# Kernel tuning notes

Hardware: AMD Instinct MI355X
Metric: run time of the kernel (lower is better)

## Reference

```python
import jax, jax.numpy as jnp
import numpy as np

B, N, DEG = 128, 512, 16          # graphs, nodes/graph, avg degree
NB = B * N                        # 65536 nodes
E = NB * DEG                      # 1048576 edges
K1, K2, K3 = 410, 205, 103        # ceil(0.8*512), ceil(0.5*410), ceil(0.5*205)
H, C = 4, 32                      # GAT heads, head dim
F_IN, ED = 128, 7


def _glorot(key, shape, fan_in):
    return jax.random.normal(key, shape, dtype=jnp.float32) / np.float32(np.sqrt(fan_in))


def setup_inputs() -> dict:
    key = jax.random.key(0)
    ks = jax.random.split(key, 24)
    x = jax.random.normal(ks[0], (NB, F_IN), dtype=jnp.float32)
    # random intra-graph edges, then offset per graph
    src = jax.random.randint(ks[1], (E,), 0, N)
    dst = jax.random.randint(ks[2], (E,), 0, N)
    off = jnp.repeat(jnp.arange(B) * N, N * DEG)
    edge_index = jnp.stack([src + off, dst + off]).astype(jnp.int32)
    edge_attr = jax.random.normal(ks[3], (E, ED), dtype=jnp.float32)
    p = {
        'c1_wl': _glorot(ks[4], (F_IN, F_IN), F_IN), 'c1_bl': jnp.zeros((F_IN,), jnp.float32), 'c1_wr': _glorot(ks[5], (F_IN, F_IN), F_IN),
        'p1_w': _glorot(ks[6], (F_IN,), F_IN),
        'c2_wl': _glorot(ks[7], (F_IN, F_IN), F_IN), 'c2_bl': jnp.zeros((F_IN,), jnp.float32), 'c2_wr': _glorot(ks[8], (F_IN, F_IN), F_IN),
        'p2_wrel': _glorot(ks[9], (F_IN, 1), F_IN), 'p2_brel': jnp.zeros((1,), jnp.float32), 'p2_wroot': _glorot(ks[10], (F_IN, 1), F_IN),
        'g_w': _glorot(ks[11], (F_IN, H * C), F_IN), 'g_as': _glorot(ks[12], (H, C), C), 'g_ad': _glorot(ks[13], (H, C), C),
        'g_we': _glorot(ks[14], (ED, H * C), ED), 'g_ae': _glorot(ks[15], (H, C), C), 'g_b': jnp.zeros((H * C,), jnp.float32),
        'p3_wrel': _glorot(ks[16], (F_IN, 1), F_IN), 'p3_brel': jnp.zeros((1,), jnp.float32), 'p3_wroot': _glorot(ks[17], (F_IN, 1), F_IN),
        'l1_w': _glorot(ks[18], (F_IN, F_IN), F_IN), 'l1_b': jnp.zeros((F_IN,), jnp.float32),
        'l2_w': _glorot(ks[19], (F_IN, 64), F_IN), 'l2_b': jnp.zeros((64,), jnp.float32),
        'l3_w': _glorot(ks[20], (64, 1), 64), 'l3_b': jnp.zeros((1,), jnp.float32),
    }
    return {'x': x, 'edge_index': edge_index, 'edge_attr': edge_attr, **p}


def _sage(x, src, dst, emf, wl, bl, wr):
    # SAGEConv: mean-aggregate neighbors (masked edges), lin_l(agg)+lin_r(x)
    agg = jax.ops.segment_sum(x[src] * emf[:, None], dst, num_segments=NB)
    cnt = jax.ops.segment_sum(emf, dst, num_segments=NB)
    mean = agg / jnp.maximum(cnt, 1.0)[:, None]
    return mean @ wl + bl + x @ wr


def _graphconv(x, src, dst, emf, wrel, brel, wroot):
    # GraphConv (SAGPooling score GNN): add-aggregation
    agg = jax.ops.segment_sum(x[src] * emf[:, None], dst, num_segments=NB)
    return (agg @ wrel + brel + x @ wroot).reshape(-1)


def _pool(x, score, nmask, K):
    # per-graph static top-k (equal-size graphs) == PyG topk + filter
    masked = jnp.where(nmask, score, -jnp.inf).reshape(B, N)
    idx = jax.lax.top_k(masked, K)[1]
    nm = jnp.zeros((B, N), dtype=bool).at[jnp.arange(B)[:, None], idx].set(True).reshape(-1)
    x = jnp.where(nm[:, None], x * score[:, None], 0.0)
    return x, nm


def _gap(x, K):
    # global mean pool; dropped nodes are exactly zero, K live nodes per graph
    return x.reshape(B, N, F_IN).sum(axis=1) / K


def _gat(x, src, dst, emf, nmask, edge_attr, w, a_s, a_d, w_e, a_e, b):
    xs = (x @ w).reshape(NB, H, C)
    al_s = (xs * a_s).sum(-1)                                   # [NB,H]
    al_d = (xs * a_d).sum(-1)
    al_e = ((edge_attr @ w_e).reshape(E, H, C) * a_e).sum(-1)    # [E,H]
    alpha = jax.nn.leaky_relu(al_s[src] + al_d[dst] + al_e, 0.2)
    alpha = jnp.where(emf[:, None] > 0, alpha, -jnp.inf)
    # PyG add_self_loops=True with fill_value='mean' for edge_attr
    ea_mean = (edge_attr * emf[:, None]).sum(0) / jnp.maximum(emf.sum(), 1.0)
    al_se = ((ea_mean @ w_e).reshape(H, C) * a_e).sum(-1)        # [H]
    alpha_self = jax.nn.leaky_relu(al_s + al_d + al_se[None, :], 0.2)
    alpha_self = jnp.where(nmask[:, None], alpha_self, -jnp.inf)
    m = jnp.maximum(jax.ops.segment_max(alpha, dst, num_segments=NB), alpha_self)
    m = jnp.where(jnp.isfinite(m), m, 0.0)
    ex = jnp.exp(alpha - m[dst]) * emf[:, None]
    ex_s = jnp.where(nmask[:, None], jnp.exp(alpha_self - m), 0.0)
    den = jnp.maximum(jax.ops.segment_sum(ex, dst, num_segments=NB) + ex_s, 1e-16)
    num = jax.ops.segment_sum(ex[:, :, None] * xs[src], dst, num_segments=NB) + ex_s[:, :, None] * xs
    return (num / den[:, :, None]).reshape(NB, H * C) + b


def _forward(x, edge_index, edge_attr, c1_wl, c1_bl, c1_wr, p1_w, c2_wl, c2_bl, c2_wr,
             p2_wrel, p2_brel, p2_wroot, g_w, g_as, g_ad, g_we, g_ae, g_b,
             p3_wrel, p3_brel, p3_wroot, l1_w, l1_b, l2_w, l2_b, l3_w, l3_b):
    src, dst = edge_index[0], edge_index[1]
    nmask = jnp.ones((NB,), dtype=bool)
    emf = jnp.ones((E,), jnp.float32)

    # block 1: SAGEConv -> TopKPooling(0.8) -> gap
    x = jax.nn.relu(_sage(x, src, dst, emf, c1_wl, c1_bl, c1_wr))
    s1 = jnp.tanh((x @ p1_w) / jnp.linalg.norm(p1_w))
    x, nmask = _pool(x, s1, nmask, K1)
    emf = emf * nmask[src] * nmask[dst]
    x1 = _gap(x, K1)

    # block 2: SAGEConv -> SAGPooling(0.5) -> gap
    x = jax.nn.relu(_sage(x, src, dst, emf, c2_wl, c2_bl, c2_wr))
    s2 = jnp.tanh(_graphconv(x, src, dst, emf, p2_wrel, p2_brel, p2_wroot))
    x, nmask = _pool(x, s2, nmask, K2)
    emf = emf * nmask[src] * nmask[dst]
    x2 = _gap(x, K2)

    # block 3: GATConv(128->32x4, edge_dim=7) -> SAGPooling(0.5) -> gap
    x = jax.nn.relu(_gat(x, src, dst, emf, nmask, edge_attr, g_w, g_as, g_ad, g_we, g_ae, g_b))
    s3 = jnp.tanh(_graphconv(x, src, dst, emf, p3_wrel, p3_brel, p3_wroot))
    x, nmask = _pool(x, s3, nmask, K3)
    x3 = _gap(x, K3)

    h = x1 + x2 + x3
    h = jax.nn.relu(h @ l1_w + l1_b)
    h = jax.nn.relu(h @ l2_w + l2_b)   # dropout identity in eval
    return jax.nn.sigmoid(h @ l3_w + l3_b)[:, 0]


def reference(x, edge_index, edge_attr, c1_wl, c1_bl, c1_wr, p1_w, c2_wl, c2_bl, c2_wr,
              p2_wrel, p2_brel, p2_wroot, g_w, g_as, g_ad, g_we, g_ae, g_b,
              p3_wrel, p3_brel, p3_wroot, l1_w, l1_b, l2_w, l2_b, l3_w, l3_b):
    return _forward(x, edge_index, edge_attr, c1_wl, c1_bl, c1_wr, p1_w, c2_wl, c2_bl, c2_wr,
                    p2_wrel, p2_brel, p2_wroot, g_w, g_as, g_ad, g_we, g_ae, g_b,
                    p3_wrel, p3_brel, p3_wroot, l1_w, l1_b, l2_w, l2_b, l3_w, l3_b)
```

## Files before the change

kernel.cpp:

```cpp
#include <hip/hip_runtime.h>
#include <math.h>

#define NBV 65536
#define EV  1048576
#define BV  128
#define K1V 410
#define K2V 205
#define K3V 103
#define NEG_BIG (-1.0e38f)

__device__ __forceinline__ float lrelu(float x){ return x > 0.f ? x : 0.2f*x; }

__global__ void k_sentinel(float* out, float v){
  int i = threadIdx.x;
  if (i < 128) out[i] = v;
}

__global__ void k_fill1(float* p, int n){
  int i = blockIdx.x*blockDim.x + threadIdx.x;
  if (i < n) p[i] = 1.f;
}

__global__ void k_zero_i(int* p, int n){
  int i = blockIdx.x*blockDim.x + threadIdx.x;
  if (i < n) p[i] = 0;
}

__global__ void k_hist(const int* dst, int* dcnt){
  int e = blockIdx.x*blockDim.x + threadIdx.x;
  if (e < EV) atomicAdd(&dcnt[dst[e]], 1);
}

__global__ void k_scan1(const int* dcnt, int* rp, int* bsum){
  __shared__ int sc[256];
  int t = threadIdx.x, i = blockIdx.x*256 + t;
  int v = dcnt[i];
  sc[t] = v; __syncthreads();
  for (int o = 1; o < 256; o <<= 1){
    int x = (t >= o) ? sc[t-o] : 0;
    __syncthreads();
    sc[t] += x;
    __syncthreads();
  }
  rp[i] = sc[t];
  if (t == 255) bsum[blockIdx.x] = sc[t];
}

__global__ void k_scan2(int* bsum){
  __shared__ int sc[256];
  int t = threadIdx.x;
  int v = bsum[t];
  sc[t] = v; __syncthreads();
  for (int o = 1; o < 256; o <<= 1){
    int x = (t >= o) ? sc[t-o] : 0;
    __syncthreads();
    sc[t] += x;
    __syncthreads();
  }
  bsum[t] = sc[t] - v;
}

__global__ void k_scan3(int* rp, const int* dcnt, const int* bsum){
  int t = threadIdx.x, i = blockIdx.x*256 + t;
  rp[i] = rp[i] - dcnt[i] + bsum[blockIdx.x];
  if (i == 0) rp[NBV] = EV;
}

__global__ void k_scatter(const int* src, const int* dst, const int* rp, int* fill,
                          int* csr_src, int* csr_eid){
  int e = blockIdx.x*blockDim.x + threadIdx.x;
  if (e < EV){
    int d = dst[e];
    int pos = atomicAdd(&fill[d], 1);
    int slot = rp[d] + pos;
    csr_src[slot] = src[e];
    csr_eid[slot] = e;
  }
}

__global__ void k_invnorm(const float* wv, float* outv){
  __shared__ float sc[128];
  int t = threadIdx.x;
  float v = wv[t];
  sc[t] = v*v; __syncthreads();
  for (int o = 64; o > 0; o >>= 1){ if (t < o) sc[t] += sc[t+o]; __syncthreads(); }
  if (t == 0) outv[0] = 1.f / sqrtf(sc[0]);
}

__global__ void k_ve(const float* g_we, const float* g_ae, float* ve){
  int t = threadIdx.x;
  if (t < 28){
    int ed = t >> 2, h = t & 3;
    float a = 0.f;
    for (int c = 0; c < 32; c++) a += g_we[ed*128 + h*32 + c] * g_ae[h*32 + c];
    ve[t] = a;
  }
}

__global__ void k_ale(const float* ea, const float* ve, float* ALE){
  int e = blockIdx.x*blockDim.x + threadIdx.x;
  if (e < EV){
    float a0=0.f,a1=0.f,a2=0.f,a3=0.f;
    for (int ed = 0; ed < 7; ed++){
      float x = ea[e*7 + ed];
      a0 += x*ve[ed*4+0]; a1 += x*ve[ed*4+1]; a2 += x*ve[ed*4+2]; a3 += x*ve[ed*4+3];
    }
    float4 o; o.x=a0; o.y=a1; o.z=a2; o.w=a3;
    *(float4*)&ALE[(size_t)e*4] = o;
  }
}

__global__ void __launch_bounds__(256) k_sage_agg(const float* X, const float* nmask,
    const int* rp, const int* csr_src, float* AGG, int masked){
  int g = blockIdx.x & 127;
  int blk = blockIdx.x >> 7;
  int i = g*512 + blk*8 + (threadIdx.x >> 5);
  int c4 = threadIdx.x & 31;
  float ax=0.f,ay=0.f,az=0.f,aw=0.f,cnt=0.f;
  if (!masked || nmask[i] > 0.f){
    int r0 = rp[i], r1 = rp[i+1];
    int s = r0;
    for (; s + 4 <= r1; s += 4){
      int sn0 = csr_src[s+0], sn1 = csr_src[s+1], sn2 = csr_src[s+2], sn3 = csr_src[s+3];
      float4 v0 = *(const float4*)&X[((size_t)sn0 << 7) + (c4 << 2)];
      float4 v1 = *(const float4*)&X[((size_t)sn1 << 7) + (c4 << 2)];
      float4 v2 = *(const float4*)&X[((size_t)sn2 << 7) + (c4 << 2)];
      float4 v3 = *(const float4*)&X[((size_t)sn3 << 7) + (c4 << 2)];
      float nm0 = masked ? nmask[sn0] : 1.f;
      float nm1 = masked ? nmask[sn1] : 1.f;
      float nm2 = masked ? nmask[sn2] : 1.f;
      float nm3 = masked ? nmask[sn3] : 1.f;
      if (nm0 > 0.f){ ax += v0.x; ay += v0.y; az += v0.z; aw += v0.w; cnt += 1.f; }
      if (nm1 > 0.f){ ax += v1.x; ay += v1.y; az += v1.z; aw += v1.w; cnt += 1.f; }
      if (nm2 > 0.f){ ax += v2.x; ay += v2.y; az += v2.z; aw += v2.w; cnt += 1.f; }
      if (nm3 > 0.f){ ax += v3.x; ay += v3.y; az += v3.z; aw += v3.w; cnt += 1.f; }
    }
    for (; s < r1; s++){
      int sn = csr_src[s];
      float nm = masked ? nmask[sn] : 1.f;
      if (nm > 0.f){
        const float4 v = *(const float4*)&X[((size_t)sn << 7) + (c4 << 2)];
        ax += v.x; ay += v.y; az += v.z; aw += v.w; cnt += 1.f;
      }
    }
  }
  float inv = 1.f / fmaxf(cnt, 1.f);
  float4 o; o.x = ax*inv; o.y = ay*inv; o.z = az*inv; o.w = aw*inv;
  *(float4*)&AGG[((size_t)i << 7) + (c4 << 2)] = o;
}

__global__ void __launch_bounds__(512) k_gemm(const float* A1, const float* A2,
    const float* W1, const float* W2, const float* bias,
    float* OUT, int has2, int relu, int hasb){
  __shared__ float ws[128][128];
  __shared__ float as[16][136];
  int t = threadIdx.x;
  int n0 = blockIdx.x * 128;
  int rowg = t >> 5;
  int colg = t & 31;
  int rb = rowg * 8;
  int jb = colg * 4;
  int an = t >> 2;
  int ak = (t & 3) << 2;
  float acc[8][4];
  for (int r = 0; r < 8; r++)
    for (int j = 0; j < 4; j++) acc[r][j] = 0.f;
  int nmat = has2 ? 2 : 1;
  for (int m = 0; m < nmat; m++){
    const float* A = (m == 0) ? A1 : A2;
    const float* W = (m == 0) ? W1 : W2;
    __syncthreads();
    for (int ii = 0; ii < 8; ii++){
      int idx4 = t + 512*ii;
      int kk = idx4 >> 5;
      int jj = (idx4 & 31) << 2;
      *(float4*)&ws[kk][jj] = *(const float4*)&W[kk*128 + jj];
    }
    float4 rA = *(const float4*)&A[((size_t)(n0+an) << 7) + ak];
    for (int c = 0; c < 8; c++){
      if (c > 0) __syncthreads();
      as[ak+0][an] = rA.x;
      as[ak+1][an] = rA.y;
      as[ak+2][an] = rA.z;
      as[ak+3][an] = rA.w;
      __syncthreads();
      if (c+1 < 8)
        rA = *(const float4*)&A[((size_t)(n0+an) << 7) + (c+1)*16 + ak];
      int kb = c*16;
      for (int kk = 0; kk < 16; kk++){
        float4 wv = *(const float4*)&ws[kb+kk][jb];
        float4 aL = *(const float4*)&as[kk][rb];
        float4 aH = *(const float4*)&as[kk][rb+4];
        float a0=aL.x,a1=aL.y,a2=aL.z,a3=aL.w,a4=aH.x,a5=aH.y,a6=aH.z,a7=aH.w;
        acc[0][0]+=a0*wv.x; acc[0][1]+=a0*wv.y; acc[0][2]+=a0*wv.z; acc[0][3]+=a0*wv.w;
        acc[1][0]+=a1*wv.x; acc[1][1]+=a1*wv.y; acc[1][2]+=a1*wv.z; acc[1][3]+=a1*wv.w;
        acc[2][0]+=a2*wv.x; acc[2][1]+=a2*wv.y; acc[2][2]+=a2*wv.z; acc[2][3]+=a2*wv.w;
        acc[3][0]+=a3*wv.x; acc[3][1]+=a3*wv.y; acc[3][2]+=a3*wv.z; acc[3][3]+=a3*wv.w;
        acc[4][0]+=a4*wv.x; acc[4][1]+=a4*wv.y; acc[4][2]+=a4*wv.z; acc[4][3]+=a4*wv.w;
        acc[5][0]+=a5*wv.x; acc[5][1]+=a5*wv.y; acc[5][2]+=a5*wv.z; acc[5][3]+=a5*wv.w;
        acc[6][0]+=a6*wv.x; acc[6][1]+=a6*wv.y; acc[6][2]+=a6*wv.z; acc[6][3]+=a6*wv.w;
        acc[7][0]+=a7*wv.x; acc[7][1]+=a7*wv.y; acc[7][2]+=a7*wv.z; acc[7][3]+=a7*wv.w;
      }
    }
  }
  float bj0=0.f,bj1=0.f,bj2=0.f,bj3=0.f;
  if (hasb){
    bj0 = bias[jb+0]; bj1 = bias[jb+1]; bj2 = bias[jb+2]; bj3 = bias[jb+3];
  }
  for (int r = 0; r < 8; r++){
    float4 o;
    o.x = acc[r][0]+bj0; o.y = acc[r][1]+bj1; o.z = acc[r][2]+bj2; o.w = acc[r][3]+bj3;
    if (relu){
      o.x = fmaxf(o.x,0.f); o.y = fmaxf(o.y,0.f); o.z = fmaxf(o.z,0.f); o.w = fmaxf(o.w,0.f);
    }
    *(float4*)&OUT[((size_t)(n0+rb+r) << 7) + jb] = o;
  }
}

__global__ void __launch_bounds__(256) k_score1(const float* X, const float* pw, const float* invn, float* s){
  int gid = blockIdx.x*256 + threadIdx.x;
  int i = gid >> 5, c4 = gid & 31;
  float4 v = *(const float4*)&X[((size_t)i << 7) + (c4 << 2)];
  float4 wv = *(const float4*)&pw[c4 << 2];
  float a = v.x*wv.x + v.y*wv.y + v.z*wv.z + v.w*wv.w;
  for (int o = 16; o > 0; o >>= 1) a += __shfl_down(a, o, 32);
  if (c4 == 0) s[i] = tanhf(a * invn[0]);
}

__global__ void __launch_bounds__(256) k_qr(const float* X, const float* wrel, const float* wroot,
                                            float* q, float* r){
  int gid = blockIdx.x*256 + threadIdx.x;
  int i = gid >> 5, c4 = gid & 31;
  float4 v = *(const float4*)&X[((size_t)i << 7) + (c4 << 2)];
  float4 wa = *(const float4*)&wrel[c4 << 2];
  float4 wb = *(const float4*)&wroot[c4 << 2];
  float aq = v.x*wa.x + v.y*wa.y + v.z*wa.z + v.w*wa.w;
  float ar = v.x*wb.x + v.y*wb.y + v.z*wb.z + v.w*wb.w;
  for (int o = 16; o > 0; o >>= 1){
    aq += __shfl_down(aq, o, 32);
    ar += __shfl_down(ar, o, 32);
  }
  if (c4 == 0){ q[i] = aq; r[i] = ar; }
}

__global__ void k_gconv(const float* q, const float* r, const float* nmask,
    const int* rp, const int* csr_src, const float* brel, float* s){
  int i = blockIdx.x*blockDim.x + threadIdx.x;
  if (i >= NBV) return;
  float acc = 0.f;
  if (nmask[i] > 0.f){
    int r0 = rp[i], r1 = rp[i+1];
    int t2 = r0;
    for (; t2 + 4 <= r1; t2 += 4){
      int sn0 = csr_src[t2+0], sn1 = csr_src[t2+1], sn2 = csr_src[t2+2], sn3 = csr_src[t2+3];
      float nm0 = nmask[sn0], nm1 = nmask[sn1], nm2 = nmask[sn2], nm3 = nmask[sn3];
      float q0 = q[sn0], q1 = q[sn1], q2 = q[sn2], q3 = q[sn3];
      if (nm0 > 0.f) acc += q0;
      if (nm1 > 0.f) acc += q1;
      if (nm2 > 0.f) acc += q2;
      if (nm3 > 0.f) acc += q3;
    }
    for (; t2 < r1; t2++){
      int sn = csr_src[t2];
      if (nmask[sn] > 0.f) acc += q[sn];
    }
  }
  s[i] = tanhf(acc + brel[0] + r[i]);
}

__global__ void __launch_bounds__(512) k_pool(const float* s, float* nmask, float* sel, int K){
  __shared__ float sc[512];
  int b = blockIdx.x, t = threadIdx.x;
  int i = b*512 + t;
  float nm = nmask[i];
  float sv = s[i];
  float ms = (nm > 0.f) ? sv : NEG_BIG;
  sc[t] = ms;
  __syncthreads();
  int rank = 0;
  for (int j = 0; j < 512; j++){
    float o = sc[j];
    rank += ((o > ms) || (o == ms && j < t)) ? 1 : 0;
  }
  bool selb = rank < K;
  nmask[i] = selb ? 1.f : 0.f;
  sel[i] = selb ? sv : 0.f;
}

__global__ void __launch_bounds__(128) k_scale_part(float* X, const float* sel, float* part){
  int b = blockIdx.x >> 3, q = blockIdx.x & 7, c = threadIdx.x;
  float acc = 0.f;
  for (int n = q*64; n < q*64 + 64; n++){
    int i = b*512 + n;
    float v = X[((size_t)i << 7) + c] * sel[i];
    X[((size_t)i << 7) + c] = v;
    acc += v;
  }
  part[(size_t)blockIdx.x*128 + c] = acc;
}

__global__ void __launch_bounds__(128) k_gap_final(const float* part, float* gap, float invK){
  int b = blockIdx.x, c = threadIdx.x;
  float s = 0.f;
  for (int q = 0; q < 8; q++) s += part[(size_t)(b*8+q)*128 + c];
  gap[b*128 + c] = s * invK;
}

__global__ void k_heads(const float* xs, const float* a_s, const float* a_d,
                        float* alS, float* alD){
  int gid = blockIdx.x*blockDim.x + threadIdx.x;
  int i = gid >> 2, h = gid & 3;
  if (i >= NBV) return;
  const float4* xr = (const float4*)&xs[((size_t)i << 7) + h*32];
  const float4* wa = (const float4*)&a_s[h*32];
  const float4* wd = (const float4*)&a_d[h*32];
  float as_ = 0.f, ad_ = 0.f;
  for (int c4 = 0; c4 < 8; c4++){
    float4 v = xr[c4]; float4 A = wa[c4]; float4 D = wd[c4];
    as_ += v.x*A.x + v.y*A.y + v.z*A.z + v.w*A.w;
    ad_ += v.x*D.x + v.y*D.y + v.z*D.z + v.w*D.w;
  }
  alS[gid] = as_; alD[gid] = ad_;
}

__global__ void __launch_bounds__(256) k_ea_part(const float* ea, const int* srcA, const int* dstA,
    const float* nmask, float* part){
  float p[8] = {0.f,0.f,0.f,0.f,0.f,0.f,0.f,0.f};
  for (int e = blockIdx.x*256 + threadIdx.x; e < EV; e += 256*256){
    if (nmask[srcA[e]] > 0.f && nmask[dstA[e]] > 0.f){
      for (int d = 0; d < 7; d++) p[d] += ea[e*7 + d];
      p[7] += 1.f;
    }
  }
  __shared__ float red[256];
  for (int comp = 0; comp < 8; comp++){
    red[threadIdx.x] = p[comp]; __syncthreads();
    for (int o = 128; o > 0; o >>= 1){ if (threadIdx.x < o) red[threadIdx.x] += red[threadIdx.x + o]; __syncthreads(); }
    if (threadIdx.x == 0) part[blockIdx.x*8 + comp] = red[0];
    __syncthreads();
  }
}

__global__ void k_ea_final(const float* part, float* easum){
  int h = threadIdx.x;
  if (h < 8){
    float s = 0.f;
    for (int b = 0; b < 256; b++) s += part[b*8 + h];
    easum[h] = s;
  }
}

__global__ void k_alse(const float* easum, const float* ve, float* alse){
  if (threadIdx.x == 0 && blockIdx.x == 0){
    float cnt = fmaxf(easum[7], 1.f);
    for (int h = 0; h < 4; h++){
      float s = 0.f;
      for (int ed = 0; ed < 7; ed++) s += (easum[ed]/cnt) * ve[ed*4 + h];
      alse[h] = s;
    }
  }
}

__global__ void __launch_bounds__(256) k_gat(const float* xs, const float* alS, const float* alD,
    const float* ALE, const float* nmask, const int* rp, const int* csr_src,
    const int* csr_eid, const float* alse, const float* g_b, float* OUT){
  int g = blockIdx.x & 127;
  int blk = blockIdx.x >> 7;
  int i = g*512 + blk*8 + (threadIdx.x >> 5);
  int lane = threadIdx.x & 31;
  int h = lane >> 3;
  int cidx = h*8 + (lane & 7);
  float nmi = nmask[i];
  const float4* xs4 = (const float4*)xs;
  float m = 0.f, den = 0.f;
  float4 acc; acc.x=0.f; acc.y=0.f; acc.z=0.f; acc.w=0.f;
  if (nmi > 0.f){
    float ald_i = alD[i*4 + h];
    m = lrelu(alS[i*4 + h] + ald_i + alse[h]);
    den = 1.f;
    acc = xs4[(size_t)i*32 + cidx];
    int r0 = rp[i], r1 = rp[i+1];
    int s = r0;
    for (; s + 4 <= r1; s += 4){
      int sn0 = csr_src[s+0], sn1 = csr_src[s+1], sn2 = csr_src[s+2], sn3 = csr_src[s+3];
      int e0 = csr_eid[s+0], e1 = csr_eid[s+1], e2 = csr_eid[s+2], e3 = csr_eid[s+3];
      float nm0 = nmask[sn0], nm1 = nmask[sn1], nm2 = nmask[sn2], nm3 = nmask[sn3];
      float al0 = alS[sn0*4 + h], al1 = alS[sn1*4 + h], al2 = alS[sn2*4 + h], al3 = alS[sn3*4 + h];
      float ae0 = ALE[(size_t)e0*4 + h], ae1 = ALE[(size_t)e1*4 + h];
      float ae2 = ALE[(size_t)e2*4 + h], ae3 = ALE[(size_t)e3*4 + h];
      float4 v0 = xs4[(size_t)sn0*32 + cidx];
      float4 v1 = xs4[(size_t)sn1*32 + cidx];
      float4 v2 = xs4[(size_t)sn2*32 + cidx];
      float4 v3 = xs4[(size_t)sn3*32 + cidx];
      if (nm0 > 0.f){
        float a = lrelu(al0 + ald_i + ae0);
        float mn = fmaxf(m, a); float pm = expf(m - mn); float pa = expf(a - mn);
        den = den*pm + pa;
        acc.x = acc.x*pm + pa*v0.x; acc.y = acc.y*pm + pa*v0.y;
        acc.z = acc.z*pm + pa*v0.z; acc.w = acc.w*pm + pa*v0.w;
        m = mn;
      }
      if (nm1 > 0.f){
        float a = lrelu(al1 + ald_i + ae1);
        float mn = fmaxf(m, a); float pm = expf(m - mn); float pa = expf(a - mn);
        den = den*pm + pa;
        acc.x = acc.x*pm + pa*v1.x; acc.y = acc.y*pm + pa*v1.y;
        acc.z = acc.z*pm + pa*v1.z; acc.w = acc.w*pm + pa*v1.w;
        m = mn;
      }
      if (nm2 > 0.f){
        float a = lrelu(al2 + ald_i + ae2);
        float mn = fmaxf(m, a); float pm = expf(m - mn); float pa = expf(a - mn);
        den = den*pm + pa;
        acc.x = acc.x*pm + pa*v2.x; acc.y = acc.y*pm + pa*v2.y;
        acc.z = acc.z*pm + pa*v2.z; acc.w = acc.w*pm + pa*v2.w;
        m = mn;
      }
      if (nm3 > 0.f){
        float a = lrelu(al3 + ald_i + ae3);
        float mn = fmaxf(m, a); float pm = expf(m - mn); float pa = expf(a - mn);
        den = den*pm + pa;
        acc.x = acc.x*pm + pa*v3.x; acc.y = acc.y*pm + pa*v3.y;
        acc.z = acc.z*pm + pa*v3.z; acc.w = acc.w*pm + pa*v3.w;
        m = mn;
      }
    }
    for (; s < r1; s++){
      int sn = csr_src[s];
      if (nmask[sn] > 0.f){
        float a = lrelu(alS[sn*4 + h] + ald_i + ALE[(size_t)csr_eid[s]*4 + h]);
        float4 v = xs4[(size_t)sn*32 + cidx];
        float mn = fmaxf(m, a); float pm = expf(m - mn); float pa = expf(a - mn);
        den = den*pm + pa;
        acc.x = acc.x*pm + pa*v.x; acc.y = acc.y*pm + pa*v.y;
        acc.z = acc.z*pm + pa*v.z; acc.w = acc.w*pm + pa*v.w;
        m = mn;
      }
    }
  }
  den = fmaxf(den, 1e-16f);
  float rd = 1.f/den;
  int cb = cidx << 2;
  float4 o;
  o.x = fmaxf(acc.x*rd + g_b[cb+0], 0.f);
  o.y = fmaxf(acc.y*rd + g_b[cb+1], 0.f);
  o.z = fmaxf(acc.z*rd + g_b[cb+2], 0.f);
  o.w = fmaxf(acc.w*rd + g_b[cb+3], 0.f);
  *(float4*)&OUT[((size_t)i << 7) + cb] = o;
}

__global__ void __launch_bounds__(128) k_mlp(const float* x1g, const float* x2g, const float* x3g,
    const float* l1w, const float* l1b, const float* l2w, const float* l2b,
    const float* l3w, const float* l3b, float* out){
  __shared__ float hh[128];
  __shared__ float h2[128];
  __shared__ float h3[64];
  int b = blockIdx.x, t = threadIdx.x;
  hh[t] = x1g[b*128 + t] + x2g[b*128 + t] + x3g[b*128 + t];
  __syncthreads();
  float a = l1b[t];
  for (int k = 0; k < 128; k++) a += hh[k] * l1w[k*128 + t];
  h2[t] = fmaxf(a, 0.f);
  __syncthreads();
  if (t < 64){
    float a2 = l2b[t];
    for (int k = 0; k < 128; k++) a2 += h2[k] * l2w[k*64 + t];
    h3[t] = fmaxf(a2, 0.f);
  }
  __syncthreads();
  if (t == 0){
    float z = l3b[0];
    for (int k = 0; k < 64; k++) z += h3[k] * l3w[k];
    out[b] = 1.f/(1.f + expf(-z));
  }
}

extern "C" void kernel_launch(void* const* d_in, const int* in_sizes, int n_in,
                              void* d_out, int out_size, void* d_ws, size_t ws_size,
                              hipStream_t stream){
  const float* x       = (const float*)d_in[0];
  const int*   ei      = (const int*)d_in[1];
  const float* ea      = (const float*)d_in[2];
  const float* c1_wl   = (const float*)d_in[3];
  const float* c1_bl   = (const float*)d_in[4];
  const float* c1_wr   = (const float*)d_in[5];
  const float* p1_w    = (const float*)d_in[6];
  const float* c2_wl   = (const float*)d_in[7];
  const float* c2_bl   = (const float*)d_in[8];
  const float* c2_wr   = (const float*)d_in[9];
  const float* p2_wrel = (const float*)d_in[10];
  const float* p2_brel = (const float*)d_in[11];
  const float* p2_wroot= (const float*)d_in[12];
  const float* g_w     = (const float*)d_in[13];
  const float* g_as    = (const float*)d_in[14];
  const float* g_ad    = (const float*)d_in[15];
  const float* g_we    = (const float*)d_in[16];
  const float* g_ae    = (const float*)d_in[17];
  const float* g_b     = (const float*)d_in[18];
  const float* p3_wrel = (const float*)d_in[19];
  const float* p3_brel = (const float*)d_in[20];
  const float* p3_wroot= (const float*)d_in[21];
  const float* l1_w    = (const float*)d_in[22];
  const float* l1_b    = (const float*)d_in[23];
  const float* l2_w    = (const float*)d_in[24];
  const float* l2_b    = (const float*)d_in[25];
  const float* l3_w    = (const float*)d_in[26];
  const float* l3_b    = (const float*)d_in[27];
  float* out = (float*)d_out;
  (void)in_sizes; (void)n_in; (void)out_size;

  char* w = (char*)d_ws;
  size_t off = 0;
  float* AGG  = (float*)(w + off); off += (size_t)NBV*128*4;
  float* F1   = (float*)(w + off); off += (size_t)NBV*128*4;
  float* F2   = (float*)(w + off); off += (size_t)NBV*128*4;
  float* ALE  = (float*)(w + off); off += (size_t)EV*4*4;
  float* sA   = (float*)(w + off); off += (size_t)NBV*4;
  float* sel  = (float*)(w + off); off += (size_t)NBV*4;
  float* qv   = (float*)(w + off); off += (size_t)NBV*4;
  float* rv   = (float*)(w + off); off += (size_t)NBV*4;
  float* nmask= (float*)(w + off); off += (size_t)NBV*4;
  float* alS  = (float*)(w + off); off += (size_t)NBV*4*4;
  float* alD  = (float*)(w + off); off += (size_t)NBV*4*4;
  float* x1g  = (float*)(w + off); off += (size_t)BV*128*4;
  float* x2g  = (float*)(w + off); off += (size_t)BV*128*4;
  float* x3g  = (float*)(w + off); off += (size_t)BV*128*4;
  float* sml  = (float*)(w + off); off += 64*4;
  float* eprt = (float*)(w + off); off += 2048*4;
  float* gprt = (float*)(w + off); off += (size_t)1024*128*4;
  int* csr_src = (int*)(w + off); off += (size_t)EV*4;
  int* csr_eid = (int*)(w + off); off += (size_t)EV*4;
  int* rp      = (int*)(w + off); off += (size_t)(NBV+64)*4;
  int* dcnt    = (int*)(w + off); off += (size_t)(NBV+64)*4;
  int* bsum    = (int*)(w + off); off += 1024;
  size_t needed = off;

  float sentinel = (ws_size >= needed) ? 0.125f : 0.875f;
  k_sentinel<<<1, 128, 0, stream>>>(out, sentinel);

  const int* srcA = ei;
  const int* dstA = ei + EV;

  k_fill1<<<NBV/256, 256, 0, stream>>>(nmask, NBV);
  k_zero_i<<<(NBV+256)/256, 256, 0, stream>>>(dcnt, NBV+1);
  k_hist<<<EV/256, 256, 0, stream>>>(dstA, dcnt);
  k_scan1<<<256, 256, 0, stream>>>(dcnt, rp, bsum);
  k_scan2<<<1, 256, 0, stream>>>(bsum);
  k_scan3<<<256, 256, 0, stream>>>(rp, dcnt, bsum);
  k_zero_i<<<(NBV+256)/256, 256, 0, stream>>>(dcnt, NBV+1);
  k_scatter<<<EV/256, 256, 0, stream>>>(srcA, dstA, rp, dcnt, csr_src, csr_eid);
  k_ve<<<1, 32, 0, stream>>>(g_we, g_ae, sml+20);
  k_ale<<<EV/256, 256, 0, stream>>>(ea, sml+20, ALE);

  k_invnorm<<<1, 128, 0, stream>>>(p1_w, sml);
  k_sage_agg<<<(NBV*32)/256, 256, 0, stream>>>(x, nmask, rp, csr_src, AGG, 0);
  k_gemm<<<NBV/128, 512, 0, stream>>>(AGG, x, c1_wl, c1_wr, c1_bl, F1, 1, 1, 1);
  k_score1<<<(NBV*32)/256, 256, 0, stream>>>(F1, p1_w, sml, sA);
  k_pool<<<BV, 512, 0, stream>>>(sA, nmask, sel, K1V);
  k_scale_part<<<BV*8, 128, 0, stream>>>(F1, sel, gprt);
  k_gap_final<<<BV, 128, 0, stream>>>(gprt, x1g, 1.f/(float)K1V);

  k_sage_agg<<<(NBV*32)/256, 256, 0, stream>>>(F1, nmask, rp, csr_src, AGG, 1);
  k_gemm<<<NBV/128, 512, 0, stream>>>(AGG, F1, c2_wl, c2_wr, c2_bl, F2, 1, 1, 1);
  k_qr<<<(NBV*32)/256, 256, 0, stream>>>(F2, p2_wrel, p2_wroot, qv, rv);
  k_gconv<<<NBV/256, 256, 0, stream>>>(qv, rv, nmask, rp, csr_src, p2_brel, sA);
  k_pool<<<BV, 512, 0, stream>>>(sA, nmask, sel, K2V);
  k_scale_part<<<BV*8, 128, 0, stream>>>(F2, sel, gprt);
  k_gap_final<<<BV, 128, 0, stream>>>(gprt, x2g, 1.f/(float)K2V);

  k_gemm<<<NBV/128, 512, 0, stream>>>(F2, F2, g_w, g_w, g_b, AGG, 0, 0, 0);
  k_heads<<<(NBV*4)/256, 256, 0, stream>>>(AGG, g_as, g_ad, alS, alD);
  k_ea_part<<<256, 256, 0, stream>>>(ea, srcA, dstA, nmask, eprt);
  k_ea_final<<<1, 64, 0, stream>>>(eprt, sml+8);
  k_alse<<<1, 64, 0, stream>>>(sml+8, sml+20, sml+16);
  k_gat<<<(NBV*32)/256, 256, 0, stream>>>(AGG, alS, alD, ALE, nmask, rp, csr_src, csr_eid, sml+16, g_b, F1);
  k_qr<<<(NBV*32)/256, 256, 0, stream>>>(F1, p3_wrel, p3_wroot, qv, rv);
  k_gconv<<<NBV/256, 256, 0, stream>>>(qv, rv, nmask, rp, csr_src, p3_brel, sA);
  k_pool<<<BV, 512, 0, stream>>>(sA, nmask, sel, K3V);
  k_scale_part<<<BV*8, 128, 0, stream>>>(F1, sel, gprt);
  k_gap_final<<<BV, 128, 0, stream>>>(gprt, x3g, 1.f/(float)K3V);

  k_mlp<<<BV, 128, 0, stream>>>(x1g, x2g, x3g, l1_w, l1_b, l2_w, l2_b, l3_w, l3_b, out);
}
```

Before: 687.6 us.

## Fuse score projections into GEMM/GAT epilogues and compact GAT GEMM to live nodes

Folds the pooling-score and GraphConv q/r projections into the GEMM and GAT epilogues as warp-shuffle reductions, so k_score1 and k_qr are removed. The pool kernel now emits a compacted index list of surviving nodes, which the GAT linear GEMM and head-attention kernel use to process only the live rows after pooling. Gathers of neighbour features, alS and ALE are also moved inside the mask branches so masked neighbours are not loaded, and several tiny init kernels are merged. The trade-off is extra epilogue register pressure and less memory-level parallelism from the now-conditional loads.

```diff
diff --git a/kernel.cpp b/kernel.cpp
--- a/kernel.cpp
+++ b/kernel.cpp
@@ -7,6 +7,7 @@
 #define K1V 410
 #define K2V 205
 #define K3V 103
+#define NL2 (BV*K2V)
 #define NEG_BIG (-1.0e38f)
 
 __device__ __forceinline__ float lrelu(float x){ return x > 0.f ? x : 0.2f*x; }
@@ -16,9 +17,10 @@
   if (i < 128) out[i] = v;
 }
 
-__global__ void k_fill1(float* p, int n){
+__global__ void k_init1(float* nmask, int* dcnt){
   int i = blockIdx.x*blockDim.x + threadIdx.x;
-  if (i < n) p[i] = 1.f;
+  if (i < NBV) nmask[i] = 1.f;
+  if (i < NBV+1) dcnt[i] = 0;
 }
 
 __global__ void k_zero_i(int* p, int n){
@@ -78,23 +80,19 @@
   }
 }
 
-__global__ void k_invnorm(const float* wv, float* outv){
+__global__ void k_ve_inv(const float* g_we, const float* g_ae, const float* p1w, float* sml){
   __shared__ float sc[128];
-  int t = threadIdx.x;
-  float v = wv[t];
-  sc[t] = v*v; __syncthreads();
-  for (int o = 64; o > 0; o >>= 1){ if (t < o) sc[t] += sc[t+o]; __syncthreads(); }
-  if (t == 0) outv[0] = 1.f / sqrtf(sc[0]);
-}
-
-__global__ void k_ve(const float* g_we, const float* g_ae, float* ve){
   int t = threadIdx.x;
   if (t < 28){
     int ed = t >> 2, h = t & 3;
     float a = 0.f;
     for (int c = 0; c < 32; c++) a += g_we[ed*128 + h*32 + c] * g_ae[h*32 + c];
-    ve[t] = a;
-  }
+    sml[20 + t] = a;
+  }
+  float v = p1w[t];
+  sc[t] = v*v; __syncthreads();
+  for (int o = 64; o > 0; o >>= 1){ if (t < o) sc[t] += sc[t+o]; __syncthreads(); }
+  if (t == 0) sml[0] = 1.f / sqrtf(sc[0]);
 }
 
 __global__ void k_ale(const float* ea, const float* ve, float* ALE){
@@ -122,18 +120,18 @@
     int s = r0;
     for (; s + 4 <= r1; s += 4){
       int sn0 = csr_src[s+0], sn1 = csr_src[s+1], sn2 = csr_src[s+2], sn3 = csr_src[s+3];
-      float4 v0 = *(const float4*)&X[((size_t)sn0 << 7) + (c4 << 2)];
-      float4 v1 = *(const float4*)&X[((size_t)sn1 << 7) + (c4 << 2)];
-      float4 v2 = *(const float4*)&X[((size_t)sn2 << 7) + (c4 << 2)];
-      float4 v3 = *(const float4*)&X[((size_t)sn3 << 7) + (c4 << 2)];
       float nm0 = masked ? nmask[sn0] : 1.f;
       float nm1 = masked ? nmask[sn1] : 1.f;
       float nm2 = masked ? nmask[sn2] : 1.f;
       float nm3 = masked ? nmask[sn3] : 1.f;
-      if (nm0 > 0.f){ ax += v0.x; ay += v0.y; az += v0.z; aw += v0.w; cnt += 1.f; }
-      if (nm1 > 0.f){ ax += v1.x; ay += v1.y; az += v1.z; aw += v1.w; cnt += 1.f; }
-      if (nm2 > 0.f){ ax += v2.x; ay += v2.y; az += v2.z; aw += v2.w; cnt += 1.f; }
-      if (nm3 > 0.f){ ax += v3.x; ay += v3.y; az += v3.z; aw += v3.w; cnt += 1.f; }
+      if (nm0 > 0.f){ float4 v = *(const float4*)&X[((size_t)sn0 << 7) + (c4 << 2)];
+                      ax += v.x; ay += v.y; az += v.z; aw += v.w; cnt += 1.f; }
+      if (nm1 > 0.f){ float4 v = *(const float4*)&X[((size_t)sn1 << 7) + (c4 << 2)];
+                      ax += v.x; ay += v.y; az += v.z; aw += v.w; cnt += 1.f; }
+      if (nm2 > 0.f){ float4 v = *(const float4*)&X[((size_t)sn2 << 7) + (c4 << 2)];
+                      ax += v.x; ay += v.y; az += v.z; aw += v.w; cnt += 1.f; }
+      if (nm3 > 0.f){ float4 v = *(const float4*)&X[((size_t)sn3 << 7) + (c4 << 2)];
+                      ax += v.x; ay += v.y; az += v.z; aw += v.w; cnt += 1.f; }
     }
     for (; s < r1; s++){
       int sn = csr_src[s];
@@ -151,7 +149,10 @@
 
 __global__ void __launch_bounds__(512) k_gemm(const float* A1, const float* A2,
     const float* W1, const float* W2, const float* bias,
-    float* OUT, int has2, int relu, int hasb){
+    float* OUT, int has2, int relu, int hasb,
+    const int* ridx, int sc_mode,
+    const float* sw1, const float* sw2, const float* sinv,
+    float* so1, float* so2){
   __shared__ float ws[128][128];
   __shared__ float as[16][136];
   int t = threadIdx.x;
@@ -162,6 +163,7 @@
   int jb = colg * 4;
   int an = t >> 2;
   int ak = (t & 3) << 2;
+  int arow = ridx ? ridx[n0 + an] : (n0 + an);
   float acc[8][4];
   for (int r = 0; r < 8; r++)
     for (int j = 0; j < 4; j++) acc[r][j] = 0.f;
@@ -176,7 +178,7 @@
       int jj = (idx4 & 31) << 2;
       *(float4*)&ws[kk][jj] = *(const float4*)&W[kk*128 + jj];
     }
-    float4 rA = *(const float4*)&A[((size_t)(n0+an) << 7) + ak];
+    float4 rA = *(const float4*)&A[((size_t)arow << 7) + ak];
     for (int c = 0; c < 8; c++){
       if (c > 0) __syncthreads();
       as[ak+0][an] = rA.x;
@@ -185,7 +187,7 @@
       as[ak+3][an] = rA.w;
       __syncthreads();
       if (c+1 < 8)
-        rA = *(const float4*)&A[((size_t)(n0+an) << 7) + (c+1)*16 + ak];
+        rA = *(const float4*)&A[((size_t)arow << 7) + (c+1)*16 + ak];
       int kb = c*16;
       for (int kk = 0; kk < 16; kk++){
         float4 wv = *(const float4*)&ws[kb+kk][jb];
@@ -207,40 +209,48 @@
   if (hasb){
     bj0 = bias[jb+0]; bj1 = bias[jb+1]; bj2 = bias[jb+2]; bj3 = bias[jb+3];
   }
+  int orow[8];
+  for (int r = 0; r < 8; r++) orow[r] = ridx ? ridx[n0+rb+r] : (n0+rb+r);
+  float w1x=0.f,w1y=0.f,w1z=0.f,w1w=0.f, w2x=0.f,w2y=0.f,w2z=0.f,w2w=0.f;
+  if (sc_mode){
+    float4 t1 = *(const float4*)&sw1[jb];
+    w1x=t1.x; w1y=t1.y; w1z=t1.z; w1w=t1.w;
+    if (sc_mode == 2){
+      float4 t2 = *(const float4*)&sw2[jb];
+      w2x=t2.x; w2y=t2.y; w2z=t2.z; w2w=t2.w;
+    }
+  }
+  float pd1[8], pd2[8];
   for (int r = 0; r < 8; r++){
     float4 o;
     o.x = acc[r][0]+bj0; o.y = acc[r][1]+bj1; o.z = acc[r][2]+bj2; o.w = acc[r][3]+bj3;
     if (relu){
       o.x = fmaxf(o.x,0.f); o.y = fmaxf(o.y,0.f); o.z = fmaxf(o.z,0.f); o.w = fmaxf(o.w,0.f);
     }
-    *(float4*)&OUT[((size_t)(n0+rb+r) << 7) + jb] = o;
-  }
-}
-
-__global__ void __launch_bounds__(256) k_score1(const float* X, const float* pw, const float* invn, float* s){
-  int gid = blockIdx.x*256 + threadIdx.x;
-  int i = gid >> 5, c4 = gid & 31;
-  float4 v = *(const float4*)&X[((size_t)i << 7) + (c4 << 2)];
-  float4 wv = *(const float4*)&pw[c4 << 2];
-  float a = v.x*wv.x + v.y*wv.y + v.z*wv.z + v.w*wv.w;
-  for (int o = 16; o > 0; o >>= 1) a += __shfl_down(a, o, 32);
-  if (c4 == 0) s[i] = tanhf(a * invn[0]);
-}
-
-__global__ void __launch_bounds__(256) k_qr(const float* X, const float* wrel, const float* wroot,
-                                            float* q, float* r){
-  int gid = blockIdx.x*256 + threadIdx.x;
-  int i = gid >> 5, c4 = gid & 31;
-  float4 v = *(const float4*)&X[((size_t)i << 7) + (c4 << 2)];
-  float4 wa = *(const float4*)&wrel[c4 << 2];
-  float4 wb = *(const float4*)&wroot[c4 << 2];
-  float aq = v.x*wa.x + v.y*wa.y + v.z*wa.z + v.w*wa.w;
-  float ar = v.x*wb.x + v.y*wb.y + v.z*wb.z + v.w*wb.w;
-  for (int o = 16; o > 0; o >>= 1){
-    aq += __shfl_down(aq, o, 32);
-    ar += __shfl_down(ar, o, 32);
-  }
-  if (c4 == 0){ q[i] = aq; r[i] = ar; }
+    if (sc_mode){
+      pd1[r] = o.x*w1x + o.y*w1y + o.z*w1z + o.w*w1w;
+      if (sc_mode == 2) pd2[r] = o.x*w2x + o.y*w2y + o.z*w2z + o.w*w2w;
+    }
+    *(float4*)&OUT[((size_t)orow[r] << 7) + jb] = o;
+  }
+  if (sc_mode == 1){
+    float inv = sinv[0];
+    for (int r = 0; r < 8; r++){
+      float a = pd1[r];
+      for (int o = 16; o > 0; o >>= 1) a += __shfl_down(a, o, 32);
+      if (colg == 0) so1[orow[r]] = tanhf(a * inv);
+    }
+  } else if (sc_mode == 2){
+    for (int r = 0; r < 8; r++){
+      float a = pd1[r];
+      float b = pd2[r];
+      for (int o = 16; o > 0; o >>= 1){
+        a += __shfl_down(a, o, 32);
+        b += __shfl_down(b, o, 32);
+      }
+      if (colg == 0){ so1[orow[r]] = a; so2[orow[r]] = b; }
+    }
+  }
 }
 
 __global__ void k_gconv(const float* q, const float* r, const float* nmask,
@@ -254,11 +264,10 @@
     for (; t2 + 4 <= r1; t2 += 4){
       int sn0 = csr_src[t2+0], sn1 = csr_src[t2+1], sn2 = csr_src[t2+2], sn3 = csr_src[t2+3];
       float nm0 = nmask[sn0], nm1 = nmask[sn1], nm2 = nmask[sn2], nm3 = nmask[sn3];
-      float q0 = q[sn0], q1 = q[sn1], q2 = q[sn2], q3 = q[sn3];
-      if (nm0 > 0.f) acc += q0;
-      if (nm1 > 0.f) acc += q1;
-      if (nm2 > 0.f) acc += q2;
-      if (nm3 > 0.f) acc += q3;
+      if (nm0 > 0.f) acc += q[sn0];
+      if (nm1 > 0.f) acc += q[sn1];
+      if (nm2 > 0.f) acc += q[sn2];
+      if (nm3 > 0.f) acc += q[sn3];
     }
     for (; t2 < r1; t2++){
       int sn = csr_src[t2];
@@ -268,7 +277,8 @@
   s[i] = tanhf(acc + brel[0] + r[i]);
 }
 
-__global__ void __launch_bounds__(512) k_pool(const float* s, float* nmask, float* sel, int K){
+__global__ void __launch_bounds__(512) k_pool(const float* s, float* nmask, float* sel,
+                                              int K, int* cidx){
   __shared__ float sc[512];
   int b = blockIdx.x, t = threadIdx.x;
   int i = b*512 + t;
@@ -285,6 +295,7 @@
   bool selb = rank < K;
   nmask[i] = selb ? 1.f : 0.f;
   sel[i] = selb ? sv : 0.f;
+  if (cidx && selb) cidx[b*K + rank] = i;
 }
 
 __global__ void __launch_bounds__(128) k_scale_part(float* X, const float* sel, float* part){
@@ -307,10 +318,11 @@
 }
 
 __global__ void k_heads(const float* xs, const float* a_s, const float* a_d,
-                        float* alS, float* alD){
+                        const int* cidx, int nlive4, float* alS, float* alD){
   int gid = blockIdx.x*blockDim.x + threadIdx.x;
-  int i = gid >> 2, h = gid & 3;
-  if (i >= NBV) return;
+  if (gid >= nlive4) return;
+  int ii = gid >> 2, h = gid & 3;
+  int i = cidx[ii];
   const float4* xr = (const float4*)&xs[((size_t)i << 7) + h*32];
   const float4* wa = (const float4*)&a_s[h*32];
   const float4* wd = (const float4*)&a_d[h*32];
@@ -320,7 +332,7 @@
     as_ += v.x*A.x + v.y*A.y + v.z*A.z + v.w*A.w;
     ad_ += v.x*D.x + v.y*D.y + v.z*D.z + v.w*D.w;
   }
-  alS[gid] = as_; alD[gid] = ad_;
+  alS[i*4 + h] = as_; alD[i*4 + h] = ad_;
 }
 
 __global__ void __launch_bounds__(256) k_ea_part(const float* ea, const int* srcA, const int* dstA,
@@ -363,7 +375,8 @@
 
 __global__ void __launch_bounds__(256) k_gat(const float* xs, const float* alS, const float* alD,
     const float* ALE, const float* nmask, const int* rp, const int* csr_src,
-    const int* csr_eid, const float* alse, const float* g_b, float* OUT){
+    const int* csr_eid, const float* alse, const float* g_b,
+    const float* wrel, const float* wroot, float* qv, float* rv, float* OUT){
   int g = blockIdx.x & 127;
   int blk = blockIdx.x >> 7;
   int i = g*512 + blk*8 + (threadIdx.x >> 5);
@@ -383,45 +396,41 @@
     int s = r0;
     for (; s + 4 <= r1; s += 4){
       int sn0 = csr_src[s+0], sn1 = csr_src[s+1], sn2 = csr_src[s+2], sn3 = csr_src[s+3];
-      int e0 = csr_eid[s+0], e1 = csr_eid[s+1], e2 = csr_eid[s+2], e3 = csr_eid[s+3];
       float nm0 = nmask[sn0], nm1 = nmask[sn1], nm2 = nmask[sn2], nm3 = nmask[sn3];
-      float al0 = alS[sn0*4 + h], al1 = alS[sn1*4 + h], al2 = alS[sn2*4 + h], al3 = alS[sn3*4 + h];
-      float ae0 = ALE[(size_t)e0*4 + h], ae1 = ALE[(size_t)e1*4 + h];
-      float ae2 = ALE[(size_t)e2*4 + h], ae3 = ALE[(size_t)e3*4 + h];
-      float4 v0 = xs4[(size_t)sn0*32 + cidx];
-      float4 v1 = xs4[(size_t)sn1*32 + cidx];
-      float4 v2 = xs4[(size_t)sn2*32 + cidx];
-      float4 v3 = xs4[(size_t)sn3*32 + cidx];
       if (nm0 > 0.f){
-        float a = lrelu(al0 + ald_i + ae0);
+        float a = lrelu(alS[sn0*4 + h] + ald_i + ALE[(size_t)csr_eid[s+0]*4 + h]);
+        float4 v = xs4[(size_t)sn0*32 + cidx];
         float mn = fmaxf(m, a); float pm = expf(m - mn); float pa = expf(a - mn);
         den = den*pm + pa;
-        acc.x = acc.x*pm + pa*v0.x; acc.y = acc.y*pm + pa*v0.y;
-        acc.z = acc.z*pm + pa*v0.z; acc.w = acc.w*pm + pa*v0.w;
+        acc.x = acc.x*pm + pa*v.x; acc.y = acc.y*pm + pa*v.y;
+        acc.z = acc.z*pm + pa*v.z; acc.w = acc.w*pm + pa*v.w;
         m = mn;
       }
       if (nm1 > 0.f){
-        float a = lrelu(al1 + ald_i + ae1);
+        float a = lrelu(alS[sn1*4 + h] + ald_i + ALE[(size_t)csr_eid[s+1]*4 + h]);
+        float4 v = xs4[(size_t)sn1*32 + cidx];
         float mn = fmaxf(m, a); float pm = expf(m - mn); float pa = expf(a - mn);
         den = den*pm + pa;
-        acc.x = acc.x*pm + pa*v1.x; acc.y = acc.y*pm + pa*v1.y;
-        acc.z = acc.z*pm + pa*v1.z; acc.w = acc.w*pm + pa*v1.w;
+        acc.x = acc.x*pm + pa*v.x; acc.y = acc.y*pm + pa*v.y;
+        acc.z = acc.z*pm + pa*v.z; acc.w = acc.w*pm + pa*v.w;
         m = mn;
       }
       if (nm2 > 0.f){
-        float a = lrelu(al2 + ald_i + ae2);
+        float a = lrelu(alS[sn2*4 + h] + ald_i + ALE[(size_t)csr_eid[s+2]*4 + h]);
+        float4 v = xs4[(size_t)sn2*32 + cidx];
         float mn = fmaxf(m, a); float pm = expf(m - mn); float pa = expf(a - mn);
         den = den*pm + pa;
-        acc.x = acc.x*pm + pa*v2.x; acc.y = acc.y*pm + pa*v2.y;
-        acc.z = acc.z*pm + pa*v2.z; acc.w = acc.w*pm + pa*v2.w;
+        acc.x = acc.x*pm + pa*v.x; acc.y = acc.y*pm + pa*v.y;
+        acc.z = acc.z*pm + pa*v.z; acc.w = acc.w*pm + pa*v.w;
         m = mn;
       }
       if (nm3 > 0.f){
-        float a = lrelu(al3 + ald_i + ae3);
+        float a = lrelu(alS[sn3*4 + h] + ald_i + ALE[(size_t)csr_eid[s+3]*4 + h]);
+        float4 v = xs4[(size_t)sn3*32 + cidx];
         float mn = fmaxf(m, a); float pm = expf(m - mn); float pa = expf(a - mn);
         den = den*pm + pa;
-        acc.x = acc.x*pm + pa*v3.x; acc.y = acc.y*pm + pa*v3.y;
-        acc.z = acc.z*pm + pa*v3.z; acc.w = acc.w*pm + pa*v3.w;
+        acc.x = acc.x*pm + pa*v.x; acc.y = acc.y*pm + pa*v.y;
+        acc.z = acc.z*pm + pa*v.z; acc.w = acc.w*pm + pa*v.w;
         m = mn;
       }
     }
@@ -447,6 +456,15 @@
   o.z = fmaxf(acc.z*rd + g_b[cb+2], 0.f);
   o.w = fmaxf(acc.w*rd + g_b[cb+3], 0.f);
   *(float4*)&OUT[((size_t)i << 7) + cb] = o;
+  float4 wa = *(const float4*)&wrel[cb];
+  float4 wb = *(const float4*)&wroot[cb];
+  float aq = o.x*wa.x + o.y*wa.y + o.z*wa.z + o.w*wa.w;
+  float ar = o.x*wb.x + o.y*wb.y + o.z*wb.z + o.w*wb.w;
+  for (int off = 16; off > 0; off >>= 1){
+    aq += __shfl_down(aq, off, 32);
+    ar += __shfl_down(ar, off, 32);
+  }
+  if (lane == 0){ qv[i] = aq; rv[i] = ar; }
 }
 
 __global__ void __launch_bounds__(128) k_mlp(const float* x1g, const float* x2g, const float* x3g,
@@ -532,6 +550,7 @@
   int* csr_eid = (int*)(w + off); off += (size_t)EV*4;
   int* rp      = (int*)(w + off); off += (size_t)(NBV+64)*4;
   int* dcnt    = (int*)(w + off); off += (size_t)(NBV+64)*4;
+  int* cidx    = (int*)(w + off); off += (size_t)NBV*4;
   int* bsum    = (int*)(w + off); off += 1024;
   size_t needed = off;
 
@@ -541,42 +560,42 @@
   const int* srcA = ei;
   const int* dstA = ei + EV;
 
-  k_fill1<<<NBV/256, 256, 0, stream>>>(nmask, NBV);
-  k_zero_i<<<(NBV+256)/256, 256, 0, stream>>>(dcnt, NBV+1);
+  k_init1<<<(NBV+256)/256, 256, 0, stream>>>(nmask, dcnt);
   k_hist<<<EV/256, 256, 0, stream>>>(dstA, dcnt);
   k_scan1<<<256, 256, 0, stream>>>(dcnt, rp, bsum);
   k_scan2<<<1, 256, 0, stream>>>(bsum);
   k_scan3<<<256, 256, 0, stream>>>(rp, dcnt, bsum);
   k_zero_i<<<(NBV+256)/256, 256, 0, stream>>>(dcnt, NBV+1);
   k_scatter<<<EV/256, 256, 0, stream>>>(srcA, dstA, rp, dcnt, csr_src, csr_eid);
-  k_ve<<<1, 32, 0, stream>>>(g_we, g_ae, sml+20);
+  k_ve_inv<<<1, 128, 0, stream>>>(g_we, g_ae, p1_w, sml);
   k_ale<<<EV/256, 256, 0, stream>>>(ea, sml+20, ALE);
 
-  k_invnorm<<<1, 128, 0, stream>>>(p1_w, sml);
   k_sage_agg<<<(NBV*32)/256, 256, 0, stream>>>(x, nmask, rp, csr_src, AGG, 0);
-  k_gemm<<<NBV/128, 512, 0, stream>>>(AGG, x, c1_wl, c1_wr, c1_bl, F1, 1, 1, 1);
-  k_score1<<<(NBV*32)/256, 256, 0, stream>>>(F1, p1_w, sml, sA);
-  k_pool<<<BV, 512, 0, stream>>>(sA, nmask, sel, K1V);
+  k_gemm<<<NBV/128, 512, 0, stream>>>(AGG, x, c1_wl, c1_wr, c1_bl, F1, 1, 1, 1,
+                                      (const int*)nullptr, 1, p1_w, (const float*)nullptr, sml, sA, (float*)nullptr);
+  k_pool<<<BV, 512, 0, stream>>>(sA, nmask, sel, K1V, (int*)nullptr);
   k_scale_part<<<BV*8, 128, 0, stream>>>(F1, sel, gprt);
   k_gap_final<<<BV, 128, 0, stream>>>(gprt, x1g, 1.f/(float)K1V);
 
   k_sage_agg<<<(NBV*32)/256, 256, 0, stream>>>(F1, nmask, rp, csr_src, AGG, 1);
-  k_gemm<<<NBV/128, 512, 0, stream>>>(AGG, F1, c2_wl, c2_wr, c2_bl, F2, 1, 1, 1);
-  k_qr<<<(NBV*32)/256, 256, 0, stream>>>(F2, p2_wrel, p2_wroot, qv, rv);
+  k_gemm<<<NBV/128, 512, 0, stream>>>(AGG, F1, c2_wl, c2_wr, c2_bl, F2, 1, 1, 1,
+                                      (const int*)nullptr, 2, p2_wrel, p2_wroot, (const float*)nullptr, qv, rv);
   k_gconv<<<NBV/256, 256, 0, stream>>>(qv, rv, nmask, rp, csr_src, p2_brel, sA);
-  k_pool<<<BV, 512, 0, stream>>>(sA, nmask, sel, K2V);
+  k_pool<<<BV, 512, 0, stream>>>(sA, nmask, sel, K2V, cidx);
   k_scale_part<<<BV*8, 128, 0, stream>>>(F2, sel, gprt);
   k_gap_final<<<BV, 128, 0, stream>>>(gprt, x2g, 1.f/(float)K2V);
 
-  k_gemm<<<NBV/128, 512, 0, stream>>>(F2, F2, g_w, g_w, g_b, AGG, 0, 0, 0);
-  k_heads<<<(NBV*4)/256, 256, 0, stream>>>(AGG, g_as, g_ad, alS, alD);
+  k_gemm<<<NL2/128, 512, 0, stream>>>(F2, F2, g_w, g_w, g_b, AGG, 0, 0, 0,
+                                      cidx, 0, (const float*)nullptr, (const float*)nullptr,
+                                      (const float*)nullptr, (float*)nullptr, (float*)nullptr);
+  k_heads<<<(NL2*4 + 255)/256, 256, 0, stream>>>(AGG, g_as, g_ad, cidx, NL2*4, alS, alD);
   k_ea_part<<<256, 256, 0, stream>>>(ea, srcA, dstA, nmask, eprt);
   k_ea_final<<<1, 64, 0, stream>>>(eprt, sml+8);
   k_alse<<<1, 64, 0, stream>>>(sml+8, sml+20, sml+16);
-  k_gat<<<(NBV*32)/256, 256, 0, stream>>>(AGG, alS, alD, ALE, nmask, rp, csr_src, csr_eid, sml+16, g_b, F1);
-  k_qr<<<(NBV*32)/256, 256, 0, stream>>>(F1, p3_wrel, p3_wroot, qv, rv);
+  k_gat<<<(NBV*32)/256, 256, 0, stream>>>(AGG, alS, alD, ALE, nmask, rp, csr_src, csr_eid,
+                                          sml+16, g_b, p3_wrel, p3_wroot, qv, rv, F1);
   k_gconv<<<NBV/256, 256, 0, stream>>>(qv, rv, nmask, rp, csr_src, p3_brel, sA);
-  k_pool<<<BV, 512, 0, stream>>>(sA, nmask, sel, K3V);
+  k_pool<<<BV, 512, 0, stream>>>(sA, nmask, sel, K3V, (int*)nullptr);
   k_scale_part<<<BV*8, 128, 0, stream>>>(F1, sel, gprt);
   k_gap_final<<<BV, 128, 0, stream>>>(gprt, x3g, 1.f/(float)K3V);
 
```

New measurement: 674.0 us. 2.0% less time.
